# Kernel optimization log

Hardware: AMD Instinct MI355X
Metric: run time of the kernel (lower is better)

## Reference

```python
import math
import jax, jax.numpy as jnp
import numpy as np

B, T, C, H = 4, 2048, 1024, 16
D = C // H  # head dim = 64


def setup_inputs() -> dict:
    key = jax.random.key(0)
    k1, k2, k3 = jax.random.split(key, 3)
    scale = 1.0 / math.sqrt(C)
    return {
        "x": jax.random.normal(k1, (B, T, C), jnp.float32),
        "w_attn": jax.random.normal(k2, (C, 3 * C), jnp.float32) * scale,
        "b_attn": jnp.zeros((3 * C,), jnp.float32),
        "w_proj": jax.random.normal(k3, (C, C), jnp.float32) * scale,
        "b_proj": jnp.zeros((C,), jnp.float32),
    }


def reference(x, w_attn, b_attn, w_proj, b_proj):
    Bx, Tx, Cx = x.shape
    qkv = x @ w_attn + b_attn                       # [B,T,3C]
    q, k, v = jnp.split(qkv, 3, axis=-1)
    # [B,T,C] -> [B,H,T,D]
    q = q.reshape(Bx, Tx, H, D).transpose(0, 2, 1, 3)
    k = k.reshape(Bx, Tx, H, D).transpose(0, 2, 1, 3)
    v = v.reshape(Bx, Tx, H, D).transpose(0, 2, 1, 3)
    att = jnp.einsum('bhqd,bhkd->bhqk', q, k) * (1.0 / math.sqrt(D))
    causal = jnp.tril(jnp.ones((Tx, Tx), bool))     # [T,T]
    att = jnp.where(causal, att, -jnp.inf)
    att = jax.nn.softmax(att, axis=-1)
    y = jnp.einsum('bhqk,bhkd->bhqd', att, v)       # [B,H,T,D]
    y = y.transpose(0, 2, 1, 3).reshape(Bx, Tx, Cx)
    return y @ w_proj + b_proj
```

## Files before the change

### kernel.cpp

```cpp
#include <hip/hip_runtime.h>
#include <hip/hip_bf16.h>

typedef __bf16 bf16;
typedef __attribute__((ext_vector_type(4))) __bf16 bf16x4;
typedef __attribute__((ext_vector_type(8))) __bf16 bf16x8;
typedef __attribute__((ext_vector_type(4))) float f32x4;
typedef __attribute__((ext_vector_type(16))) float f32x16;
typedef __attribute__((ext_vector_type(2))) unsigned u32x2;
typedef __attribute__((ext_vector_type(4))) unsigned u32x4;

#define B_ 4
#define T_ 2048
#define C_ 1024
#define H_ 16
#define D_ 64
#define BT_ (B_*T_)

#define NEG_INF (-__builtin_inff())

__device__ __forceinline__ void gld16(const void* g, void* l) {
  __builtin_amdgcn_global_load_lds(
      (const __attribute__((address_space(1))) void*)g,
      (__attribute__((address_space(3))) void*)l, 16, 0, 0);
}

__device__ __forceinline__ unsigned cvtpk(float lo, float hi) {
  unsigned r;
  asm("v_cvt_pk_bf16_f32 %0, %1, %2" : "=v"(r) : "v"(lo), "v"(hi));
  return r;
}


__global__ void cast_x(const float* __restrict__ in, bf16* __restrict__ out) {
  int i = blockIdx.x * 256 + threadIdx.x;
  f32x4 v = reinterpret_cast<const f32x4*>(in)[i];
  bf16x4 o;
  o[0] = (bf16)v[0]; o[1] = (bf16)v[1]; o[2] = (bf16)v[2]; o[3] = (bf16)v[3];
  reinterpret_cast<bf16x4*>(out)[i] = o;
}

__global__ void transpose_cast(const float* __restrict__ in, bf16* __restrict__ out,
                               int R, int Cc) {
  __shared__ float tile[32][33];
  int tx = threadIdx.x, ty = threadIdx.y;
  int x  = blockIdx.x * 32 + tx;
  int y0 = blockIdx.y * 32;
#pragma unroll
  for (int j = 0; j < 32; j += 8)
    tile[ty + j][tx] = in[(size_t)(y0 + ty + j) * Cc + x];
  __syncthreads();
  int ox  = y0 + tx;
  int oy0 = blockIdx.x * 32;
#pragma unroll
  for (int j = 0; j < 32; j += 8)
    out[(size_t)(oy0 + ty + j) * R + ox] = (bf16)tile[tx][ty + j];
}


template<int EPI>
__global__ __launch_bounds__(256)
void gemm_bt(const bf16* __restrict__ A, const bf16* __restrict__ Bt,
             const float* __restrict__ bias, float* __restrict__ outF,
             bf16* __restrict__ qb, bf16* __restrict__ kb, bf16* __restrict__ vb,
             int M, int N, int K) {
  __shared__ alignas(16) bf16 As[128 * 32];
  __shared__ alignas(16) bf16 Bs[128 * 32];
  const int tid = threadIdx.x;
  const int lane = tid & 63, wid = tid >> 6;
  const int wm = wid >> 1, wn = wid & 1;
  const int lr = lane & 15, lg = lane >> 4;
  const int m0 = blockIdx.y * 128, n0 = blockIdx.x * 128;

  f32x4 acc[4][4] = {};

  const int ktiles = K >> 5;
  for (int kt = 0; kt < ktiles; ++kt) {
    const int k0 = kt << 5;
#pragma unroll
    for (int j = 0; j < 2; ++j) {
      int s = j * 256 + tid;
      int row = s >> 2, ke = (s & 3) << 3;
      gld16(A  + (size_t)(m0 + row) * K + k0 + ke, As + s * 8);
      gld16(Bt + (size_t)(n0 + row) * K + k0 + ke, Bs + s * 8);
    }
    __syncthreads();
    bf16x8 af[4], bfr[4];
#pragma unroll
    for (int i = 0; i < 4; i++)
      af[i]  = *(const bf16x8*)(As + ((wm * 64 + i * 16 + lr) << 5) + (lg << 3));
#pragma unroll
    for (int i = 0; i < 4; i++)
      bfr[i] = *(const bf16x8*)(Bs + ((wn * 64 + i * 16 + lr) << 5) + (lg << 3));
#pragma unroll
    for (int i = 0; i < 4; i++)
#pragma unroll
      for (int j = 0; j < 4; j++)
        acc[i][j] = __builtin_amdgcn_mfma_f32_16x16x32_bf16(af[i], bfr[j], acc[i][j], 0, 0, 0);
    __syncthreads();
  }

  if (EPI == 1) {
#pragma unroll
    for (int i = 0; i < 4; i++) {
      int row = m0 + wm * 64 + i * 16 + lg * 4;
#pragma unroll
      for (int j = 0; j < 4; j++) {
        int col = n0 + wn * 64 + j * 16 + lr;
        float bv = bias[col];
#pragma unroll
        for (int r = 0; r < 4; r++)
          outF[(size_t)(row + r) * N + col] = acc[i][j][r] + bv;
      }
    }
  } else {
    const int sect = n0 >> 10;
#pragma unroll
    for (int i = 0; i < 4; i++) {
      int row = m0 + wm * 64 + i * 16 + lg * 4;
#pragma unroll
      for (int j = 0; j < 4; j++) {
        int col = n0 + wn * 64 + j * 16 + lr;
        float bv = bias[col];
        int cm = col & 1023;
        int h = cm >> 6, d = cm & 63;
#pragma unroll
        for (int r = 0; r < 4; r++) {
          float v = acc[i][j][r] + bv;
          int rt = row + r;
          int b = rt >> 11, t = rt & 2047;
          bf16 o = (bf16)v;
          size_t bh = (size_t)(b * H_ + h);
          if (sect == 0)      qb[(bh * T_ + t) * D_ + d] = o;
          else if (sect == 1) kb[(bh * T_ + t) * D_ + d] = o;
          else                vb[(bh * D_ + d) * T_ + t] = o;
        }
      }
    }
  }
}


#if __has_builtin(__builtin_amdgcn_permlane32_swap)
#define PERMSWAP(A, B, LOW, HIW) do {                                           \
    auto _r = __builtin_amdgcn_permlane32_swap((unsigned)(A), (unsigned)(B),    \
                                               false, false);                   \
    __builtin_memcpy(&(LOW), &_r, 4);                                           \
    __builtin_memcpy(&(HIW), (const char*)&_r + 4, 4);                          \
  } while (0)
#else
#define PERMSWAP(A, B, LOW, HIW) do {                                           \
    unsigned _sb = (unsigned)__shfl_xor((int)(B), 32, 64);                      \
    unsigned _sa = (unsigned)__shfl_xor((int)(A), 32, 64);                      \
    (LOW) = hi ? _sb : (A);                                                     \
    (HIW) = hi ? (B) : _sa;                                                     \
  } while (0)
#endif

__global__ __launch_bounds__(256, 4)
void attn_fwd(const bf16* __restrict__ qg, const bf16* __restrict__ kg,
              const bf16* __restrict__ vg, bf16* __restrict__ yb) {
  __shared__ alignas(16) bf16 Ks[3][64 * 64];
  __shared__ alignas(16) bf16 Vs[3][64 * 64];
  const int tid = threadIdx.x;
  const int lane = tid & 63, wid = tid >> 6;
  const int hi = lane >> 5, lq = lane & 31;
  const int xr = (lq & 7) << 4;
  const int bh = blockIdx.y;
  const int NQ = T_ / 128;

  const char* kbase = (const char*)(kg + (size_t)bh * T_ * D_);
  const char* vbase = (const char*)(vg + (size_t)bh * D_ * T_);
  const int b_ = bh >> 4, h = bh & 15;

#define STAGE(BF, TT) do {                                                     \
    _Pragma("unroll")                                                          \
    for (int j_ = 0; j_ < 2; ++j_) {                                           \
      int s_ = j_ * 256 + tid;                                                 \
      int row_ = s_ >> 3;                                                      \
      int scb_ = ((s_ & 7) << 4) ^ ((row_ & 7) << 4);                          \
      gld16(kbase + (size_t)((TT) * 64 + row_) * 128 + scb_,                   \
            (char*)Ks[BF] + s_ * 16);                                          \
      gld16(vbase + (size_t)row_ * (T_ * 2) + (TT) * 128 + scb_,               \
            (char*)Vs[BF] + s_ * 16);                                          \
    }                                                                          \
  } while (0)

  for (int ph = 0; ph < 2; ++ph) {
    const int qblk = ph ? (int)blockIdx.x : (NQ - 1 - (int)blockIdx.x);
    const int wq0 = qblk * 128 + wid * 32;
    const int qrow = wq0 + lq;
    const int nt = 2 * qblk + 2;

    if (ph) __builtin_amdgcn_s_barrier();
    STAGE(0, 0);
    STAGE(1, 1);

    const bf16* qptr = qg + ((size_t)bh * T_ + qrow) * D_ + hi * 8;
    bf16x8 qf[4];
#pragma unroll
    for (int s = 0; s < 4; s++) {
      qf[s] = *(const bf16x8*)(qptr + 16 * s);
      asm volatile("" : "+v"(qf[s]));
    }

    f32x16 o[2] = {};
    float mrow = NEG_INF, lrow = 0.f;

    for (int t = 0; t < nt; ++t) {
      if (t + 1 < nt) asm volatile("s_waitcnt vmcnt(4)" ::: "memory");
      else            asm volatile("s_waitcnt vmcnt(0)" ::: "memory");
      __builtin_amdgcn_s_barrier();
      asm volatile("" ::: "memory");
      if (t + 2 < nt) STAGE((t + 2) % 3, t + 2);

      const char* Kc = (const char*)Ks[t % 3];
      const char* Vc = (const char*)Vs[t % 3];

      f32x16 S[2] = {};
      __builtin_amdgcn_s_setprio(1);
#pragma unroll
      for (int s = 0; s < 4; s++) {
#pragma unroll
        for (int b = 0; b < 2; b++) {
          bf16x8 kf = *(const bf16x8*)(Kc + (b * 32 + lq) * 128 +
                                       ((32 * s + 16 * hi) ^ xr));
          S[b] = __builtin_amdgcn_mfma_f32_32x32x16_bf16(kf, qf[s], S[b], 0, 0, 0);
        }
      }
      __builtin_amdgcn_s_setprio(0);

      if (t >= nt - 2) {
#pragma unroll
        for (int b = 0; b < 2; b++)
#pragma unroll
          for (int r = 0; r < 16; r++) {
            int kgl = t * 64 + b * 32 + (r & 3) + 8 * (r >> 2) + 4 * hi;
            if (kgl > qrow) S[b][r] = NEG_INF;
          }
      }

      float tm = NEG_INF;
#pragma unroll
      for (int b = 0; b < 2; b++)
#pragma unroll
        for (int r = 0; r < 16; r++) tm = fmaxf(tm, S[b][r]);
      tm = fmaxf(tm, __shfl_xor(tm, 32, 64));

      float mn = fmaxf(mrow, 0.125f * tm);
      float alpha = __expf(mrow - mn);
      mrow = mn;
      float rs = 0.f;
#pragma unroll
      for (int b = 0; b < 2; b++)
#pragma unroll
        for (int r = 0; r < 16; r++) {
          float e = __expf(fmaf(S[b][r], 0.125f, -mn));
          S[b][r] = e;
          rs += e;
        }
      rs += __shfl_xor(rs, 32, 64);
      lrow = lrow * alpha + rs;
#pragma unroll
      for (int db = 0; db < 2; db++)
#pragma unroll
        for (int r = 0; r < 16; r++) o[db][r] *= alpha;

      __builtin_amdgcn_s_setprio(1);
#pragma unroll
      for (int ks = 0; ks < 4; ks++) {
        const int b = ks >> 1, hf = ks & 1;
        unsigned A0 = cvtpk(S[b][8 * hf + 0], S[b][8 * hf + 1]);
        unsigned A1 = cvtpk(S[b][8 * hf + 2], S[b][8 * hf + 3]);
        unsigned B0 = cvtpk(S[b][8 * hf + 4], S[b][8 * hf + 5]);
        unsigned B1 = cvtpk(S[b][8 * hf + 6], S[b][8 * hf + 7]);
        unsigned w0, w1, w2, w3;
        PERMSWAP(A0, B0, w0, w2);
        PERMSWAP(A1, B1, w1, w3);
        u32x4 wv = {w0, w1, w2, w3};
        bf16x8 pf = __builtin_bit_cast(bf16x8, wv);
#pragma unroll
        for (int db = 0; db < 2; db++) {
          bf16x8 vf = *(const bf16x8*)(Vc + (db * 32 + lq) * 128 +
                                       ((32 * ks + 16 * hi) ^ xr));
          o[db] = __builtin_amdgcn_mfma_f32_32x32x16_bf16(vf, pf, o[db], 0, 0, 0);
        }
      }
      __builtin_amdgcn_s_setprio(0);
    }

    float inv = 1.f / lrow;
    bf16* yrow = yb + ((size_t)(b_ * T_ + qrow)) * C_ + h * 64 + hi * 4;
#pragma unroll
    for (int db = 0; db < 2; db++)
#pragma unroll
      for (int rq = 0; rq < 4; rq++) {
        unsigned w0 = cvtpk(o[db][4 * rq + 0] * inv, o[db][4 * rq + 1] * inv);
        unsigned w1 = cvtpk(o[db][4 * rq + 2] * inv, o[db][4 * rq + 3] * inv);
        u32x2 wv = {w0, w1};
        *(u32x2*)(yrow + db * 32 + rq * 8) = wv;
      }
  }
#undef STAGE
}


extern "C" void kernel_launch(void* const* d_in, const int* in_sizes, int n_in,
                              void* d_out, int out_size, void* d_ws, size_t ws_size,
                              hipStream_t stream) {
  (void)in_sizes; (void)n_in; (void)out_size; (void)ws_size;
  const float* x      = (const float*)d_in[0];
  const float* w_attn = (const float*)d_in[1];
  const float* b_attn = (const float*)d_in[2];
  const float* w_proj = (const float*)d_in[3];
  const float* b_proj = (const float*)d_in[4];
  float* out = (float*)d_out;

  char* ws = (char*)d_ws;
  bf16* x_bf = (bf16*)ws;  ws += (size_t)BT_ * C_ * 2;
  bf16* wat  = (bf16*)ws;  ws += (size_t)3 * C_ * C_ * 2;
  bf16* wpt  = (bf16*)ws;  ws += (size_t)C_ * C_ * 2;
  bf16* qbuf = (bf16*)ws;  ws += (size_t)BT_ * C_ * 2;
  bf16* kbuf = (bf16*)ws;  ws += (size_t)BT_ * C_ * 2;
  bf16* vbuf = (bf16*)ws;  ws += (size_t)BT_ * C_ * 2;
  bf16* ybuf = (bf16*)ws;

  cast_x<<<(BT_ * C_ / 4) / 256, 256, 0, stream>>>(x, x_bf);
  transpose_cast<<<dim3(3 * C_ / 32, C_ / 32), dim3(32, 8), 0, stream>>>(w_attn, wat, C_, 3 * C_);
  transpose_cast<<<dim3(C_ / 32, C_ / 32), dim3(32, 8), 0, stream>>>(w_proj, wpt, C_, C_);

  gemm_bt<0><<<dim3(3 * C_ / 128, BT_ / 128), 256, 0, stream>>>(
      x_bf, wat, b_attn, nullptr, qbuf, kbuf, vbuf, BT_, 3 * C_, C_);

  attn_fwd<<<dim3(T_ / 256, B_ * H_), 256, 0, stream>>>(qbuf, kbuf, vbuf, ybuf);

  gemm_bt<1><<<dim3(C_ / 128, BT_ / 128), 256, 0, stream>>>(
      ybuf, wpt, b_proj, out, nullptr, nullptr, nullptr, BT_, C_, C_);
}
```

Baseline: 299.5 us.

## Triple-buffer GEMM loads with 128x256 tiles, 512 threads, and block swizzle

Restructures the bf16 GEMM used for the QKV and output projections. Tiles grow to 128x256 with 8 waves per block, and global-to-LDS loads are triple-buffered with vmcnt waits so the next tiles' fetches overlap MFMA work. One barrier per k-step replaces two. A block-index swizzle groups neighbouring workgroups for better L2 reuse. This raises LDS use and register pressure, and the manual waitcnt logic depends on the exact number of outstanding loads per stage.

```diff
diff --git a/kernel.cpp b/kernel.cpp
--- a/kernel.cpp
+++ b/kernel.cpp
@@ -58,46 +58,64 @@
 
 
 template<int EPI>
-__global__ __launch_bounds__(256)
+__global__ __launch_bounds__(512, 4)
 void gemm_bt(const bf16* __restrict__ A, const bf16* __restrict__ Bt,
              const float* __restrict__ bias, float* __restrict__ outF,
              bf16* __restrict__ qb, bf16* __restrict__ kb, bf16* __restrict__ vb,
              int M, int N, int K) {
-  __shared__ alignas(16) bf16 As[128 * 32];
-  __shared__ alignas(16) bf16 Bs[128 * 32];
+  __shared__ alignas(16) bf16 As[3][128 * 32];
+  __shared__ alignas(16) bf16 Bs[3][256 * 32];
   const int tid = threadIdx.x;
   const int lane = tid & 63, wid = tid >> 6;
-  const int wm = wid >> 1, wn = wid & 1;
+  const int wm = wid >> 2, wn = wid & 3;
   const int lr = lane & 15, lg = lane >> 4;
-  const int m0 = blockIdx.y * 128, n0 = blockIdx.x * 128;
+
+  const int nbx = gridDim.x;
+  const int nwg = nbx * gridDim.y;
+  const int bid = blockIdx.y * nbx + blockIdx.x;
+  const int swz = (bid & 7) * (nwg >> 3) + (bid >> 3);
+  const int m0 = (swz / nbx) * 128, n0 = (swz % nbx) * 256;
 
   f32x4 acc[4][4] = {};
 
+#define GSTAGE(BF, KT) do {                                                    \
+    int k0_ = (KT) << 5;                                                       \
+    { int row_ = tid >> 2, ke_ = (tid & 3) << 3;                               \
+      gld16(A + (size_t)(m0 + row_) * K + k0_ + ke_, As[BF] + tid * 8); }      \
+    _Pragma("unroll")                                                          \
+    for (int j_ = 0; j_ < 2; ++j_) {                                           \
+      int s_ = j_ * 512 + tid;                                                 \
+      int row_ = s_ >> 2, ke_ = (s_ & 3) << 3;                                 \
+      gld16(Bt + (size_t)(n0 + row_) * K + k0_ + ke_, Bs[BF] + s_ * 8);        \
+    }                                                                          \
+  } while (0)
+
   const int ktiles = K >> 5;
+  GSTAGE(0, 0);
+  GSTAGE(1, 1);
   for (int kt = 0; kt < ktiles; ++kt) {
-    const int k0 = kt << 5;
-#pragma unroll
-    for (int j = 0; j < 2; ++j) {
-      int s = j * 256 + tid;
-      int row = s >> 2, ke = (s & 3) << 3;
-      gld16(A  + (size_t)(m0 + row) * K + k0 + ke, As + s * 8);
-      gld16(Bt + (size_t)(n0 + row) * K + k0 + ke, Bs + s * 8);
-    }
-    __syncthreads();
+    if (kt + 1 < ktiles) asm volatile("s_waitcnt vmcnt(3)" ::: "memory");
+    else                 asm volatile("s_waitcnt vmcnt(0)" ::: "memory");
+    __builtin_amdgcn_s_barrier();
+    asm volatile("" ::: "memory");
+    if (kt + 2 < ktiles) GSTAGE((kt + 2) % 3, kt + 2);
+
+    const bf16* Ac = As[kt % 3];
+    const bf16* Bc = Bs[kt % 3];
     bf16x8 af[4], bfr[4];
 #pragma unroll
     for (int i = 0; i < 4; i++)
-      af[i]  = *(const bf16x8*)(As + ((wm * 64 + i * 16 + lr) << 5) + (lg << 3));
-#pragma unroll
-    for (int i = 0; i < 4; i++)
-      bfr[i] = *(const bf16x8*)(Bs + ((wn * 64 + i * 16 + lr) << 5) + (lg << 3));
+      af[i]  = *(const bf16x8*)(Ac + ((wm * 64 + i * 16 + lr) << 5) + (lg << 3));
+#pragma unroll
+    for (int j = 0; j < 4; j++)
+      bfr[j] = *(const bf16x8*)(Bc + ((wn * 64 + j * 16 + lr) << 5) + (lg << 3));
 #pragma unroll
     for (int i = 0; i < 4; i++)
 #pragma unroll
       for (int j = 0; j < 4; j++)
         acc[i][j] = __builtin_amdgcn_mfma_f32_16x16x32_bf16(af[i], bfr[j], acc[i][j], 0, 0, 0);
-    __syncthreads();
   }
+#undef GSTAGE
 
   if (EPI == 1) {
 #pragma unroll
@@ -328,11 +346,11 @@
   transpose_cast<<<dim3(3 * C_ / 32, C_ / 32), dim3(32, 8), 0, stream>>>(w_attn, wat, C_, 3 * C_);
   transpose_cast<<<dim3(C_ / 32, C_ / 32), dim3(32, 8), 0, stream>>>(w_proj, wpt, C_, C_);
 
-  gemm_bt<0><<<dim3(3 * C_ / 128, BT_ / 128), 256, 0, stream>>>(
+  gemm_bt<0><<<dim3(3 * C_ / 256, BT_ / 128), 512, 0, stream>>>(
       x_bf, wat, b_attn, nullptr, qbuf, kbuf, vbuf, BT_, 3 * C_, C_);
 
   attn_fwd<<<dim3(T_ / 256, B_ * H_), 256, 0, stream>>>(qbuf, kbuf, vbuf, ybuf);
 
-  gemm_bt<1><<<dim3(C_ / 128, BT_ / 128), 256, 0, stream>>>(
+  gemm_bt<1><<<dim3(C_ / 256, BT_ / 128), 512, 0, stream>>>(
       ybuf, wpt, b_proj, out, nullptr, nullptr, nullptr, BT_, C_, C_);
 }
```

Measured after the change: 307.9 us. +2.8%, slower.
